# Optimization experiments

Hardware: AMD Instinct MI355X
Metric: run time of the kernel (lower is better)

The kernel has to match this reference:

```python
import jax, jax.numpy as jnp
import numpy as np

HEADS = 8
DIM_HEAD = 32
SCALE = DIM_HEAD ** -0.5


def _split_heads(t):
    # [b, n, h*d] -> [b, h, n, d]
    b, n, hd = t.shape
    return t.reshape(b, n, HEADS, hd // HEADS).transpose(0, 2, 1, 3)


def setup_inputs() -> dict:
    key = jax.random.key(0)
    k1, k2, k3, k4 = jax.random.split(key, 4)
    b, n, dim = 2, 2048, 256
    inner = HEADS * DIM_HEAD  # 256
    x = jax.random.normal(k1, (b, n, dim), dtype=jnp.float32)
    attn_feat = jax.random.normal(k2, (b, n, dim), dtype=jnp.float32)
    # nn.Linear(dim, 3*inner, bias=False): store as [dim, 3*inner] for x @ W
    W_qkv = jax.random.normal(k3, (dim, 3 * inner), dtype=jnp.float32) * (dim ** -0.5)
    W_qkv_aux = jax.random.normal(k4, (dim, 3 * inner), dtype=jnp.float32) * (dim ** -0.5)
    return {"x": x, "attn_feat": attn_feat, "W_qkv": W_qkv, "W_qkv_aux": W_qkv_aux,
            "use_cls_tokens": 1}


def reference(x, attn_feat, W_qkv, W_qkv_aux, use_cls_tokens):
    b, n, dim = x.shape
    # aux Q,K (v_aux computed but unused, matching original chunk of 3)
    qkv_aux = attn_feat @ W_qkv_aux            # [b, n, 3*inner]
    q_aux, k_aux, _ = jnp.split(qkv_aux, 3, axis=-1)
    q_aux, k_aux = _split_heads(q_aux), _split_heads(k_aux)
    # self Q,K
    qkv_self = x @ W_qkv
    q_self, k_self, _ = jnp.split(qkv_self, 3, axis=-1)
    q_self, k_self = _split_heads(q_self), _split_heads(k_self)
    # dual score product: (QK^T_aux * scale) * (QK^T_self * scale)
    dots_aux = jnp.einsum('bhid,bhjd->bhij', q_aux, k_aux) * SCALE
    dots_self = jnp.einsum('bhid,bhjd->bhij', q_self, k_self) * SCALE
    attn = jax.nn.softmax(dots_aux * dots_self, axis=-1)  # [b, h, n, n]
    # v = x.unsqueeze(1): broadcast raw x over heads
    out = jnp.einsum('bhij,bjd->bhid', attn, x)           # [b, h, n, dim]
    out = out.transpose(0, 2, 1, 3).reshape(b, n, HEADS * dim)
    attn_flat = attn.transpose(0, 2, 1, 3).reshape(b, n, HEADS * n)
    return (out, out[:, 0], attn_flat[:, 0])
```

## Files before the change

kernel.cpp:

```cpp
#include <hip/hip_runtime.h>

typedef _Float16 f16;
typedef _Float16 f16x4 __attribute__((ext_vector_type(4)));
typedef _Float16 f16x8 __attribute__((ext_vector_type(8)));
typedef float f32x4 __attribute__((ext_vector_type(4)));

#define LOG2E 1.4426950408889634f
#define SCL   (1.4426950408889634f / 32.0f)

__global__ __launch_bounds__(256) void k_transpose(const float* __restrict__ x,
                                                   f16* __restrict__ xt) {
  __shared__ f16 tile[64][65];
  int n0 = blockIdx.x * 64;
  int d0 = blockIdx.y * 64;
  int b  = blockIdx.z;
  int t = threadIdx.x;
  int colr = t & 63, rowg = t >> 6;
#pragma unroll
  for (int r = 0; r < 16; ++r) {
    int row = r * 4 + rowg;
    tile[row][colr] = (f16)x[((size_t)b * 2048 + n0 + row) * 256 + d0 + colr];
  }
  __syncthreads();
#pragma unroll
  for (int r = 0; r < 16; ++r) {
    int drow = r * 4 + rowg;
    xt[((size_t)b * 256 + d0 + drow) * 2048 + n0 + colr] = tile[colr][drow];
  }
}

__global__ __launch_bounds__(256) void k_transW(const float* __restrict__ Wq,
    const float* __restrict__ Wa, f16* __restrict__ Wt) {
  __shared__ f16 tile[64][65];
  int n0 = blockIdx.x * 64, k0 = blockIdx.y * 64, s = blockIdx.z;
  const float* W = s ? Wa : Wq;
  f16* dst = Wt + (size_t)s * 512 * 256;
  int t = threadIdx.x, c = t & 63, rg = t >> 6;
#pragma unroll
  for (int r = 0; r < 16; ++r) {
    int krow = r * 4 + rg;
    tile[krow][c] = (f16)W[(size_t)(k0 + krow) * 768 + n0 + c];
  }
  __syncthreads();
#pragma unroll
  for (int r = 0; r < 16; ++r) {
    int nrow = r * 4 + rg;
    dst[(size_t)(n0 + nrow) * 256 + k0 + c] = tile[c][nrow];
  }
}

__global__ __launch_bounds__(256) void k_proj(const float* __restrict__ x,
    const float* __restrict__ af, const f16* __restrict__ Wt,
    f16* __restrict__ Qs, f16* __restrict__ Ks,
    f16* __restrict__ Qa, f16* __restrict__ Ka) {
  int mt = blockIdx.x, nt = blockIdx.y, s = blockIdx.z;
  const float* A = s ? af : x;
  const f16* W = Wt + (size_t)s * 512 * 256;
  f16* Qd = s ? Qa : Qs;
  f16* Kd = s ? Ka : Ks;
  int t = threadIdx.x, wv = t >> 6, ln = t & 63, cl = ln & 15, g = ln >> 4;
  int m0 = mt * 64, n0 = nt * 64;
  const float* arow = A + (size_t)(m0 + wv * 16 + cl) * 256 + g * 8;
  const f16* wb = W + (size_t)n0 * 256 + g * 8;
  f32x4 z4 = {0.f, 0.f, 0.f, 0.f};
  f32x4 acc[4] = {z4, z4, z4, z4};
#pragma unroll
  for (int k32 = 0; k32 < 8; ++k32) {
    float4 u = *(const float4*)(arow + k32 * 32);
    float4 v = *(const float4*)(arow + k32 * 32 + 4);
    f16x8 a = { (f16)u.x, (f16)u.y, (f16)u.z, (f16)u.w,
                (f16)v.x, (f16)v.y, (f16)v.z, (f16)v.w };
#pragma unroll
    for (int n4 = 0; n4 < 4; ++n4) {
      f16x8 bf = *(const f16x8*)(wb + (size_t)(n4 * 16 + cl) * 256 + k32 * 32);
      acc[n4] = __builtin_amdgcn_mfma_f32_16x16x32_f16(a, bf, acc[n4], 0, 0, 0);
    }
  }
#pragma unroll
  for (int n4 = 0; n4 < 4; ++n4) {
    int c = n0 + n4 * 16 + cl;
    int head = (c & 255) >> 5, d = c & 31;
    f16* dst = (c < 256) ? Qd : Kd;
#pragma unroll
    for (int r = 0; r < 4; ++r) {
      int m = m0 + wv * 16 + g * 4 + r;
      int bb = m >> 11, nn = m & 2047;
      dst[(((size_t)bb * 8 + head) * 2048 + nn) * 32 + d] = (f16)acc[n4][r];
    }
  }
}

__global__ __launch_bounds__(256) void k_flash(const f16* __restrict__ Qs,
    const f16* __restrict__ Ks, const f16* __restrict__ Qa,
    const f16* __restrict__ Ka, const f16* __restrict__ xt,
    float* __restrict__ out, float* __restrict__ out_cls) {
  __shared__ f16 KaL[2][64][40];
  __shared__ f16 KsL[2][64][40];
  __shared__ f16 PL[2][64][72];
  __shared__ float alphaL[2][64];
  __shared__ float lL[64];
  int qt = blockIdx.x, h = blockIdx.y, b = blockIdx.z;
  int bh = b * 8 + h;
  int t = threadIdx.x, wv = t >> 6, ln = t & 63, cl = ln & 15, g = ln >> 4;
  int qrow0 = qt * 64 + wv * 16;
  f16x8 qsf = *(const f16x8*)&Qs[((size_t)bh * 2048 + qrow0 + cl) * 32 + g * 8];
  f16x8 qaf = *(const f16x8*)&Qa[((size_t)bh * 2048 + qrow0 + cl) * 32 + g * 8];
  f32x4 z4 = {0.f, 0.f, 0.f, 0.f};
  f32x4 acc[4][4];
#pragma unroll
  for (int i = 0; i < 4; ++i)
#pragma unroll
    for (int j = 0; j < 4; ++j) acc[i][j] = z4;
  float m_run = -3.0e38f, l_run = 0.f;
  int krow = t >> 2, koff = (t & 3) * 8;
  const f16* kaSrc = Ka + ((size_t)bh * 2048 + krow) * 32 + koff;
  const f16* ksSrc = Ks + ((size_t)bh * 2048 + krow) * 32 + koff;
  const f16* xb = xt + ((size_t)b * 256 + wv * 64) * 2048;

  *(f16x8*)&KaL[0][krow][koff] = *(const f16x8*)kaSrc;
  *(f16x8*)&KsL[0][krow][koff] = *(const f16x8*)ksSrc;
  __syncthreads();

  for (int kt = 0; kt < 32; ++kt) {
    int buf = kt & 1;
    f16x8 kan, ksn;
    if (kt < 31) {
      kan = *(const f16x8*)(kaSrc + (size_t)(kt + 1) * 2048);
      ksn = *(const f16x8*)(ksSrc + (size_t)(kt + 1) * 2048);
    }
    f16x8 xf[2][4];
#pragma unroll
    for (int ks2 = 0; ks2 < 2; ++ks2)
#pragma unroll
      for (int ddt = 0; ddt < 4; ++ddt)
        xf[ks2][ddt] = *(const f16x8*)(xb + (size_t)(ddt * 16 + cl) * 2048 +
                                       kt * 64 + ks2 * 32 + g * 8);
    float p[16];
    float tmax = -3.0e38f;
#pragma unroll
    for (int jt = 0; jt < 4; ++jt) {
      f16x8 kaf = *(const f16x8*)&KaL[buf][jt * 16 + cl][g * 8];
      f16x8 ksf = *(const f16x8*)&KsL[buf][jt * 16 + cl][g * 8];
      f32x4 za = __builtin_amdgcn_mfma_f32_16x16x32_f16(kaf, qaf, z4, 0, 0, 0);
      f32x4 zs = __builtin_amdgcn_mfma_f32_16x16x32_f16(ksf, qsf, z4, 0, 0, 0);
#pragma unroll
      for (int r = 0; r < 4; ++r) {
        float sv = za[r] * zs[r] * SCL;
        p[jt * 4 + r] = sv;
        tmax = fmaxf(tmax, sv);
      }
    }
    tmax = fmaxf(tmax, __shfl_xor(tmax, 16, 64));
    tmax = fmaxf(tmax, __shfl_xor(tmax, 32, 64));
    float m_new = fmaxf(m_run, tmax);
    float alpha = exp2f(m_run - m_new);
    float lsum = 0.f;
#pragma unroll
    for (int q = 0; q < 16; ++q) {
      p[q] = exp2f(p[q] - m_new);
      lsum += p[q];
    }
    lsum += __shfl_xor(lsum, 16, 64);
    lsum += __shfl_xor(lsum, 32, 64);
    l_run = l_run * alpha + lsum;
    m_run = m_new;
    if (kt < 31) {
      *(f16x8*)&KaL[buf ^ 1][krow][koff] = kan;
      *(f16x8*)&KsL[buf ^ 1][krow][koff] = ksn;
    }
#pragma unroll
    for (int jt = 0; jt < 4; ++jt) {
      f16x4 pk = { (f16)p[jt * 4 + 0], (f16)p[jt * 4 + 1],
                   (f16)p[jt * 4 + 2], (f16)p[jt * 4 + 3] };
      *(f16x4*)&PL[buf][wv * 16 + cl][jt * 16 + g * 4] = pk;
    }
    if (g == 0) alphaL[buf][wv * 16 + cl] = alpha;
    __syncthreads();
    float av[4][4];
    int need = 0;
#pragma unroll
    for (int qt2 = 0; qt2 < 4; ++qt2)
#pragma unroll
      for (int r = 0; r < 4; ++r) {
        float a = alphaL[buf][qt2 * 16 + g * 4 + r];
        av[qt2][r] = a;
        need |= (a != 1.0f);
      }
    if (__any(need)) {
#pragma unroll
      for (int qt2 = 0; qt2 < 4; ++qt2)
#pragma unroll
        for (int ddt = 0; ddt < 4; ++ddt)
#pragma unroll
          for (int r = 0; r < 4; ++r) acc[qt2][ddt][r] *= av[qt2][r];
    }
#pragma unroll
    for (int ks2 = 0; ks2 < 2; ++ks2) {
      f16x8 pf[4];
#pragma unroll
      for (int qt2 = 0; qt2 < 4; ++qt2)
        pf[qt2] = *(const f16x8*)&PL[buf][qt2 * 16 + cl][ks2 * 32 + g * 8];
#pragma unroll
      for (int ddt = 0; ddt < 4; ++ddt)
#pragma unroll
        for (int qt2 = 0; qt2 < 4; ++qt2)
          acc[qt2][ddt] = __builtin_amdgcn_mfma_f32_16x16x32_f16(
              pf[qt2], xf[ks2][ddt], acc[qt2][ddt], 0, 0, 0);
    }
  }
  if (g == 0) lL[wv * 16 + cl] = l_run;
  __syncthreads();
#pragma unroll
  for (int qt2 = 0; qt2 < 4; ++qt2) {
#pragma unroll
    for (int r = 0; r < 4; ++r) {
      float linv = 1.0f / lL[qt2 * 16 + g * 4 + r];
      int q = qt * 64 + qt2 * 16 + g * 4 + r;
#pragma unroll
      for (int ddt = 0; ddt < 4; ++ddt) {
        float v = acc[qt2][ddt][r] * linv;
        int col = h * 256 + wv * 64 + ddt * 16 + cl;
        out[((size_t)b * 2048 + q) * 2048 + col] = v;
        if (q == 0) out_cls[(size_t)b * 2048 + col] = v;
      }
    }
  }
}

__global__ __launch_bounds__(256) void k_attn0(const f16* __restrict__ Qs,
    const f16* __restrict__ Ks, const f16* __restrict__ Qa,
    const f16* __restrict__ Ka, float* __restrict__ dst) {
  __shared__ float qa_s[32], qs_s[32];
  __shared__ float red[256];
  int h = blockIdx.x, b = blockIdx.y, bh = b * 8 + h;
  int t = threadIdx.x;
  if (t < 32) {
    qa_s[t] = (float)Qa[(size_t)bh * 2048 * 32 + t];
    qs_s[t] = (float)Qs[(size_t)bh * 2048 * 32 + t];
  }
  __syncthreads();
  float sv[8];
#pragma unroll
  for (int r = 0; r < 8; ++r) {
    int j = r * 256 + t;
    const f16x8* ka8 = (const f16x8*)&Ka[((size_t)bh * 2048 + j) * 32];
    const f16x8* ks8 = (const f16x8*)&Ks[((size_t)bh * 2048 + j) * 32];
    float da = 0.f, ds = 0.f;
#pragma unroll
    for (int c = 0; c < 4; ++c) {
      f16x8 va = ka8[c], vs = ks8[c];
#pragma unroll
      for (int d = 0; d < 8; ++d) {
        da += qa_s[c * 8 + d] * (float)va[d];
        ds += qs_s[c * 8 + d] * (float)vs[d];
      }
    }
    sv[r] = da * ds * (1.f / 32.f);
  }
  float mx = sv[0];
#pragma unroll
  for (int r = 1; r < 8; ++r) mx = fmaxf(mx, sv[r]);
  red[t] = mx;
  __syncthreads();
  for (int st = 128; st > 0; st >>= 1) {
    if (t < st) red[t] = fmaxf(red[t], red[t + st]);
    __syncthreads();
  }
  float m = red[0];
  __syncthreads();
  float e[8], sum = 0.f;
#pragma unroll
  for (int r = 0; r < 8; ++r) {
    e[r] = exp2f((sv[r] - m) * LOG2E);
    sum += e[r];
  }
  red[t] = sum;
  __syncthreads();
  for (int st = 128; st > 0; st >>= 1) {
    if (t < st) red[t] += red[t + st];
    __syncthreads();
  }
  float l = red[0];
#pragma unroll
  for (int r = 0; r < 8; ++r)
    dst[(size_t)b * 16384 + h * 2048 + r * 256 + t] = e[r] / l;
}

extern "C" void kernel_launch(void* const* d_in, const int* in_sizes, int n_in,
                              void* d_out, int out_size, void* d_ws, size_t ws_size,
                              hipStream_t stream) {
  const float* x  = (const float*)d_in[0];
  const float* af = (const float*)d_in[1];
  const float* Wq = (const float*)d_in[2];
  const float* Wa = (const float*)d_in[3];
  const size_t QK = (size_t)2 * 8 * 2048 * 32;
  f16* Qs = (f16*)d_ws;
  f16* Ks = Qs + QK;
  f16* Qa = Ks + QK;
  f16* Ka = Qa + QK;
  f16* xt = Ka + QK;
  f16* Wt = xt + QK;
  float* out     = (float*)d_out;
  float* out_cls = out + (size_t)2 * 2048 * 2048;
  float* attn0   = out_cls + 2 * 2048;

  k_transpose<<<dim3(32, 4, 2), 256, 0, stream>>>(x, xt);
  k_transW<<<dim3(8, 4, 2), 256, 0, stream>>>(Wq, Wa, Wt);
  k_proj<<<dim3(64, 8, 2), 256, 0, stream>>>(x, af, Wt, Qs, Ks, Qa, Ka);
  k_flash<<<dim3(32, 8, 2), 256, 0, stream>>>(Qs, Ks, Qa, Ka, xt, out, out_cls);
  k_attn0<<<dim3(8, 2), 256, 0, stream>>>(Qs, Ks, Qa, Ka, attn0);
}
```

Before: 186.6 us.

## Software-pipeline score and PV stages with lazy max rescaling in flash kernel

Restructures the flash attention loop so the score MFMAs for tile k overlap the PV MFMAs for tile k-1, leaving one barrier per iteration. Adds a lazy running-max update that rescales only when the new max exceeds the old by a threshold, plus per-wave flags that let whole quarter tiles skip the accumulator rescale. Also uses packed f16 conversion, tree reductions and a launch-bounds occupancy hint. The threshold scheme can let exponentials grow large before rescaling, and the extra live registers from pipelining may reduce occupancy.

```diff
diff --git a/kernel.cpp b/kernel.cpp
--- a/kernel.cpp
+++ b/kernel.cpp
@@ -7,6 +7,7 @@
 
 #define LOG2E 1.4426950408889634f
 #define SCL   (1.4426950408889634f / 32.0f)
+#define TH_RAW 177.445f
 
 __global__ __launch_bounds__(256) void k_transpose(const float* __restrict__ x,
                                                    f16* __restrict__ xt) {
@@ -90,14 +91,15 @@
   }
 }
 
-__global__ __launch_bounds__(256) void k_flash(const f16* __restrict__ Qs,
+__global__ __launch_bounds__(256, 2) void k_flash(const f16* __restrict__ Qs,
     const f16* __restrict__ Ks, const f16* __restrict__ Qa,
     const f16* __restrict__ Ka, const f16* __restrict__ xt,
     float* __restrict__ out, float* __restrict__ out_cls) {
   __shared__ f16 KaL[2][64][40];
   __shared__ f16 KsL[2][64][40];
   __shared__ f16 PL[2][64][72];
-  __shared__ float alphaL[2][64];
+  __shared__ float alphaL[2][64] __attribute__((aligned(16)));
+  __shared__ int   rsF[2][4] __attribute__((aligned(16)));
   __shared__ float lL[64];
   int qt = blockIdx.x, h = blockIdx.y, b = blockIdx.z;
   int bh = b * 8 + h;
@@ -117,26 +119,10 @@
   const f16* ksSrc = Ks + ((size_t)bh * 2048 + krow) * 32 + koff;
   const f16* xb = xt + ((size_t)b * 256 + wv * 64) * 2048;
 
-  *(f16x8*)&KaL[0][krow][koff] = *(const f16x8*)kaSrc;
-  *(f16x8*)&KsL[0][krow][koff] = *(const f16x8*)ksSrc;
-  __syncthreads();
-
-  for (int kt = 0; kt < 32; ++kt) {
-    int buf = kt & 1;
-    f16x8 kan, ksn;
-    if (kt < 31) {
-      kan = *(const f16x8*)(kaSrc + (size_t)(kt + 1) * 2048);
-      ksn = *(const f16x8*)(ksSrc + (size_t)(kt + 1) * 2048);
-    }
-    f16x8 xf[2][4];
-#pragma unroll
-    for (int ks2 = 0; ks2 < 2; ++ks2)
-#pragma unroll
-      for (int ddt = 0; ddt < 4; ++ddt)
-        xf[ks2][ddt] = *(const f16x8*)(xb + (size_t)(ddt * 16 + cl) * 2048 +
-                                       kt * 64 + ks2 * 32 + g * 8);
-    float p[16];
-    float tmax = -3.0e38f;
+  float tv[16];
+  f16x8 xf[2][4];
+
+  auto SCORE_MM = [&](int buf) {
 #pragma unroll
     for (int jt = 0; jt < 4; ++jt) {
       f16x8 kaf = *(const f16x8*)&KaL[buf][jt * 16 + cl][g * 8];
@@ -144,62 +130,77 @@
       f32x4 za = __builtin_amdgcn_mfma_f32_16x16x32_f16(kaf, qaf, z4, 0, 0, 0);
       f32x4 zs = __builtin_amdgcn_mfma_f32_16x16x32_f16(ksf, qsf, z4, 0, 0, 0);
 #pragma unroll
-      for (int r = 0; r < 4; ++r) {
-        float sv = za[r] * zs[r] * SCL;
-        p[jt * 4 + r] = sv;
-        tmax = fmaxf(tmax, sv);
+      for (int r = 0; r < 4; ++r) tv[jt * 4 + r] = za[r] * zs[r];
+    }
+  };
+
+  auto SCORE_FIN = [&](int buf) {
+    float a0 = fmaxf(tv[0], tv[1]),   a1 = fmaxf(tv[2], tv[3]);
+    float a2 = fmaxf(tv[4], tv[5]),   a3 = fmaxf(tv[6], tv[7]);
+    float a4 = fmaxf(tv[8], tv[9]),   a5 = fmaxf(tv[10], tv[11]);
+    float a6 = fmaxf(tv[12], tv[13]), a7 = fmaxf(tv[14], tv[15]);
+    float b0 = fmaxf(a0, a1), b1 = fmaxf(a2, a3);
+    float b2 = fmaxf(a4, a5), b3 = fmaxf(a6, a7);
+    float tm = fmaxf(fmaxf(b0, b1), fmaxf(b2, b3));
+    tm = fmaxf(tm, __shfl_xor(tm, 16, 64));
+    tm = fmaxf(tm, __shfl_xor(tm, 32, 64));
+    bool upd = tm > m_run + TH_RAW;
+    float m_new = upd ? tm : m_run;
+    float alpha = upd ? exp2f((m_run - m_new) * SCL) : 1.0f;
+    float mS = m_new * SCL;
+    float p[16];
+#pragma unroll
+    for (int i = 0; i < 16; ++i) p[i] = exp2f(fmaf(tv[i], SCL, -mS));
+    float s0 = p[0] + p[1],   s1 = p[2] + p[3];
+    float s2 = p[4] + p[5],   s3 = p[6] + p[7];
+    float s4 = p[8] + p[9],   s5 = p[10] + p[11];
+    float s6 = p[12] + p[13], s7 = p[14] + p[15];
+    float u0 = s0 + s1, u1 = s2 + s3, u2 = s4 + s5, u3 = s6 + s7;
+    float ls = (u0 + u1) + (u2 + u3);
+    ls += __shfl_xor(ls, 16, 64);
+    ls += __shfl_xor(ls, 32, 64);
+    l_run = fmaf(l_run, alpha, ls);
+    m_run = m_new;
+#pragma unroll
+    for (int jt = 0; jt < 4; ++jt) {
+      auto lo = __builtin_amdgcn_cvt_pkrtz(p[jt * 4 + 0], p[jt * 4 + 1]);
+      auto hi = __builtin_amdgcn_cvt_pkrtz(p[jt * 4 + 2], p[jt * 4 + 3]);
+      f16x4 pk = { (f16)lo[0], (f16)lo[1], (f16)hi[0], (f16)hi[1] };
+      *(f16x4*)&PL[buf][wv * 16 + cl][jt * 16 + g * 4] = pk;
+    }
+    if (g == 0) alphaL[buf][wv * 16 + cl] = alpha;
+    int wany = __any(upd) ? 1 : 0;
+    if (ln == 0) rsF[buf][wv] = wany;
+  };
+
+  auto XFLOAD = [&](int kt) {
+#pragma unroll
+    for (int ks2 = 0; ks2 < 2; ++ks2)
+#pragma unroll
+      for (int ddt = 0; ddt < 4; ++ddt)
+        xf[ks2][ddt] = *(const f16x8*)(xb + (size_t)(ddt * 16 + cl) * 2048 +
+                                       kt * 64 + ks2 * 32 + g * 8);
+  };
+
+  auto PVDO = [&](int pbuf) {
+    int4 fl = *(const int4*)&rsF[pbuf][0];
+    int flq[4] = { fl.x, fl.y, fl.z, fl.w };
+#pragma unroll
+    for (int qt2 = 0; qt2 < 4; ++qt2) {
+      if (flq[qt2]) {
+        f32x4 a4 = *(const f32x4*)&alphaL[pbuf][qt2 * 16 + g * 4];
+#pragma unroll
+        for (int ddt = 0; ddt < 4; ++ddt)
+#pragma unroll
+          for (int r = 0; r < 4; ++r) acc[qt2][ddt][r] *= a4[r];
       }
-    }
-    tmax = fmaxf(tmax, __shfl_xor(tmax, 16, 64));
-    tmax = fmaxf(tmax, __shfl_xor(tmax, 32, 64));
-    float m_new = fmaxf(m_run, tmax);
-    float alpha = exp2f(m_run - m_new);
-    float lsum = 0.f;
-#pragma unroll
-    for (int q = 0; q < 16; ++q) {
-      p[q] = exp2f(p[q] - m_new);
-      lsum += p[q];
-    }
-    lsum += __shfl_xor(lsum, 16, 64);
-    lsum += __shfl_xor(lsum, 32, 64);
-    l_run = l_run * alpha + lsum;
-    m_run = m_new;
-    if (kt < 31) {
-      *(f16x8*)&KaL[buf ^ 1][krow][koff] = kan;
-      *(f16x8*)&KsL[buf ^ 1][krow][koff] = ksn;
-    }
-#pragma unroll
-    for (int jt = 0; jt < 4; ++jt) {
-      f16x4 pk = { (f16)p[jt * 4 + 0], (f16)p[jt * 4 + 1],
-                   (f16)p[jt * 4 + 2], (f16)p[jt * 4 + 3] };
-      *(f16x4*)&PL[buf][wv * 16 + cl][jt * 16 + g * 4] = pk;
-    }
-    if (g == 0) alphaL[buf][wv * 16 + cl] = alpha;
-    __syncthreads();
-    float av[4][4];
-    int need = 0;
-#pragma unroll
-    for (int qt2 = 0; qt2 < 4; ++qt2)
-#pragma unroll
-      for (int r = 0; r < 4; ++r) {
-        float a = alphaL[buf][qt2 * 16 + g * 4 + r];
-        av[qt2][r] = a;
-        need |= (a != 1.0f);
-      }
-    if (__any(need)) {
-#pragma unroll
-      for (int qt2 = 0; qt2 < 4; ++qt2)
-#pragma unroll
-        for (int ddt = 0; ddt < 4; ++ddt)
-#pragma unroll
-          for (int r = 0; r < 4; ++r) acc[qt2][ddt][r] *= av[qt2][r];
     }
 #pragma unroll
     for (int ks2 = 0; ks2 < 2; ++ks2) {
       f16x8 pf[4];
 #pragma unroll
       for (int qt2 = 0; qt2 < 4; ++qt2)
-        pf[qt2] = *(const f16x8*)&PL[buf][qt2 * 16 + cl][ks2 * 32 + g * 8];
+        pf[qt2] = *(const f16x8*)&PL[pbuf][qt2 * 16 + cl][ks2 * 32 + g * 8];
 #pragma unroll
       for (int ddt = 0; ddt < 4; ++ddt)
 #pragma unroll
@@ -207,7 +208,40 @@
           acc[qt2][ddt] = __builtin_amdgcn_mfma_f32_16x16x32_f16(
               pf[qt2], xf[ks2][ddt], acc[qt2][ddt], 0, 0, 0);
     }
-  }
+  };
+
+  *(f16x8*)&KaL[0][krow][koff] = *(const f16x8*)kaSrc;
+  *(f16x8*)&KsL[0][krow][koff] = *(const f16x8*)ksSrc;
+  __syncthreads();
+
+  f16x8 kan = *(const f16x8*)(kaSrc + 2048);
+  f16x8 ksn = *(const f16x8*)(ksSrc + 2048);
+  SCORE_MM(0);
+  SCORE_FIN(0);
+  *(f16x8*)&KaL[1][krow][koff] = kan;
+  *(f16x8*)&KsL[1][krow][koff] = ksn;
+  __syncthreads();
+
+  for (int k = 1; k < 32; ++k) {
+    int sbuf = k & 1, pbuf = sbuf ^ 1;
+    XFLOAD(k - 1);
+    if (k < 31) {
+      kan = *(const f16x8*)(kaSrc + (size_t)(k + 1) * 2048);
+      ksn = *(const f16x8*)(ksSrc + (size_t)(k + 1) * 2048);
+    }
+    SCORE_MM(sbuf);
+    PVDO(pbuf);
+    SCORE_FIN(sbuf);
+    if (k < 31) {
+      *(f16x8*)&KaL[pbuf][krow][koff] = kan;
+      *(f16x8*)&KsL[pbuf][krow][koff] = ksn;
+    }
+    __syncthreads();
+  }
+
+  XFLOAD(31);
+  PVDO(1);
+
   if (g == 0) lL[wv * 16 + cl] = l_run;
   __syncthreads();
 #pragma unroll
```

New measurement: 178.4 us. -4.4%, faster.
